# Performance work log

Hardware: AMD Instinct MI355X
Metric: run time of the kernel (lower is better)

## Reference

```python
import jax, jax.numpy as jnp
import numpy as np

CAR_DIM = 8
ESC_MAX_AGENT = 32
HID = 256
ACTION_DIM = 30
NUM_STATES = 64
BATCH = 8192
ENC_OUT = 1 + CAR_DIM * ESC_MAX_AGENT          # 257
Q_IN = 1 + CAR_DIM + CAR_DIM * ESC_MAX_AGENT   # 265


def setup_inputs() -> dict:
    key = jax.random.key(0)
    ks = jax.random.split(key, 9)
    s = jax.random.normal(ks[0], (BATCH, CAR_DIM + NUM_STATES * CAR_DIM), dtype=jnp.float32)
    def lin(k, fan_in, fan_out):
        bound = 1.0 / np.sqrt(fan_in)
        kw, kb = jax.random.split(k)
        W = jax.random.uniform(kw, (fan_in, fan_out), jnp.float32, -bound, bound)
        b = jax.random.uniform(kb, (fan_out,), jnp.float32, -bound, bound)
        return W, b
    W1, b1 = lin(ks[1], CAR_DIM, HID)
    W2, b2 = lin(ks[2], HID, ENC_OUT)
    Qw1, Qb1 = lin(ks[3], Q_IN, HID)
    Qw2, Qb2 = lin(ks[4], HID, ACTION_DIM)
    return {"s": s, "W1": W1, "b1": b1, "W2": W2, "b2": b2,
            "Qw1": Qw1, "Qb1": Qb1, "Qw2": Qw2, "Qb2": Qb2}


def reference(s, W1, b1, W2, b2, Qw1, Qb1, Qw2, Qb2):
    B = s.shape[0]
    self_states = s[:, :CAR_DIM]                                   # [B, C]
    surr = s[:, CAR_DIM:].reshape(B, -1, CAR_DIM)                  # [B, N, C]
    # sentinel agents: any coordinate exactly == -1 is skipped
    valid = ~jnp.any(surr == -1.0, axis=-1)                        # [B, N] bool
    h = jax.nn.relu(jnp.einsum('bnc,ch->bnh', surr, W1) + b1)      # [B, N, HID]
    enc = jax.nn.relu(jnp.einsum('bnh,he->bne', h, W2) + b2)       # [B, N, ENC_OUT]
    sum_outputs = jnp.sum(enc * valid[:, :, None].astype(enc.dtype), axis=1)  # [B, ENC_OUT]
    x = jnp.concatenate([self_states, sum_outputs], axis=1)        # [B, Q_IN]
    q = jax.nn.relu(x @ Qw1 + Qb1) @ Qw2 + Qb2                     # [B, ACTION_DIM]
    return q
```

## Files before the change

kernel.cpp:

```cpp
#include <hip/hip_runtime.h>

#define CAR 8
#define SROW 520
#define HID 256
#define EOUT 257
#define XPAD 288
#define ADIM 30

typedef __attribute__((ext_vector_type(8))) short sh8;
typedef __attribute__((ext_vector_type(4))) float f32x4;

__device__ __forceinline__ short f2bf(float f) {
  unsigned u = __builtin_bit_cast(unsigned, f);
  u += 0x7fffu + ((u >> 16) & 1u);
  return (short)(u >> 16);
}
__device__ __forceinline__ unsigned f2bf2(float a, float b) {
  unsigned ua = __builtin_bit_cast(unsigned, a);
  ua += 0x7fffu + ((ua >> 16) & 1u);
  unsigned ub = __builtin_bit_cast(unsigned, b);
  ub += 0x7fffu + ((ub >> 16) & 1u);
  return __builtin_amdgcn_perm(ub, ua, 0x07060302);
}

__global__ void k_prep(const float* __restrict__ W1, const float* __restrict__ W2,
                       const float* __restrict__ Qw1, const float* __restrict__ Qw2,
                       short* __restrict__ w1f, short* __restrict__ w2f,
                       short* __restrict__ w3f, short* __restrict__ wq2f) {
  int idx = blockIdx.x * 256 + threadIdx.x;
  if (idx < 8192) {
    int mt = idx >> 9, r = idx & 511, lane = r >> 3, j = r & 7;
    int quad = lane >> 4, m = lane & 15;
    float v = (quad == 0) ? W1[j * HID + mt * 16 + m] : 0.0f;
    w1f[idx] = f2bf(v);
    return;
  }
  int i2 = idx - 8192;
  if (i2 < 69632) {
    int ks = i2 / 8704, r = i2 % 8704;
    int nt = r >> 9, r2 = r & 511, lane = r2 >> 3, j = r2 & 7;
    int quad = lane >> 4, m = lane & 15;
    int k = ks * 32 + quad * 8 + j, n = nt * 16 + m;
    float v = (n < EOUT) ? W2[k * EOUT + n] : 0.0f;
    w2f[i2] = f2bf(v);
    return;
  }
  int i3 = i2 - 69632;
  if (i3 < 73728) {
    int ks = i3 >> 13, r = i3 & 8191;
    int nt = r >> 9, r2 = r & 511, lane = r2 >> 3, j = r2 & 7;
    int quad = lane >> 4, m = lane & 15;
    int k = ks * 32 + quad * 8 + j, n = nt * 16 + m;
    float v = (k < 265) ? Qw1[k * HID + n] : 0.0f;
    w3f[i3] = f2bf(v);
    return;
  }
  int i4 = i3 - 73728;
  if (i4 < 8192) {
    int ks = i4 >> 10, r = i4 & 1023;
    int nt = r >> 9, r2 = r & 511, lane = r2 >> 3, j = r2 & 7;
    int quad = lane >> 4, m = lane & 15;
    int k = ks * 32 + quad * 8 + j, n = nt * 16 + m;
    float v = (n < ADIM) ? Qw2[k * ADIM + n] : 0.0f;
    wq2f[i4] = f2bf(v);
  }
}

__global__ __launch_bounds__(256, 2)
void k_enc(const float* __restrict__ s, const short* __restrict__ w1f,
           const float* __restrict__ b1, const short* __restrict__ w2f,
           const float* __restrict__ b2, float* __restrict__ so288) {
  __shared__ __align__(16) short hlds[2][16384];
  __shared__ float ninvp[4];

  const int tid = threadIdx.x;
  const int w = tid >> 6, lane = tid & 63;
  const int q = lane >> 4, m = lane & 15;
  const int be = w >> 1, half = w & 1;
  const size_t b0 = 2 * (size_t)blockIdx.x;
  const int bg = (int)b0 + be;

  const float* srow0 = s + (size_t)bg * SROW + CAR;
  int4 pk = {0, 0, 0, 0};
  bool inv = false;
  if (lane < 32) {
    const float* sr = srow0 + (half * 32 + lane) * CAR;
    float4 f0 = ((const float4*)sr)[0], f1 = ((const float4*)sr)[1];
    inv = (f0.x == -1.f) | (f0.y == -1.f) | (f0.z == -1.f) | (f0.w == -1.f) |
          (f1.x == -1.f) | (f1.y == -1.f) | (f1.z == -1.f) | (f1.w == -1.f);
    pk.x = (int)f2bf2(f0.x, f0.y); pk.y = (int)f2bf2(f0.z, f0.w);
    pk.z = (int)f2bf2(f1.x, f1.y); pk.w = (int)f2bf2(f1.z, f1.w);
  }
  const float vflag = inv ? 0.f : 1.f;
  unsigned long long bal = __ballot(inv);
  if (lane == 0) ninvp[w] = (float)__popcll(bal);

  int4 p0, p1;
  p0.x = __shfl(pk.x, m, 64);      p0.y = __shfl(pk.y, m, 64);
  p0.z = __shfl(pk.z, m, 64);      p0.w = __shfl(pk.w, m, 64);
  p1.x = __shfl(pk.x, 16 + m, 64); p1.y = __shfl(pk.y, 16 + m, 64);
  p1.z = __shfl(pk.z, 16 + m, 64); p1.w = __shfl(pk.w, 16 + m, 64);
  const float vv0 = __shfl(vflag, m, 64);
  const float vv1 = __shfl(vflag, 16 + m, 64);
  if (q != 0) { p0.x = p0.y = p0.z = p0.w = 0; p1.x = p1.y = p1.z = p1.w = 0; }
  sh8 bs0 = __builtin_bit_cast(sh8, p0);
  sh8 bs1 = __builtin_bit_cast(sh8, p1);

  const int T0 = half * 2, T1 = half * 2 + 1;
#pragma unroll
  for (int mt = 0; mt < 16; ++mt) {
    sh8 af = *(const sh8*)(w1f + (mt * 64 + lane) * 8);
    f32x4 z = {0.f, 0.f, 0.f, 0.f};
    f32x4 c0 = __builtin_amdgcn_mfma_f32_16x16x32_bf16(af, bs0, z, 0, 0, 0);
    f32x4 c1 = __builtin_amdgcn_mfma_f32_16x16x32_bf16(af, bs1, z, 0, 0, 0);
    const int hidb = mt * 16 + q * 4;
    float4 b1v = *(const float4*)(b1 + hidb);
    const int ks = hidb >> 5, qB = (hidb >> 3) & 3, js = hidb & 7;
    uint2 k0, k1;
    k0.x = f2bf2(fmaxf(c0[0] + b1v.x, 0.f) * vv0, fmaxf(c0[1] + b1v.y, 0.f) * vv0);
    k0.y = f2bf2(fmaxf(c0[2] + b1v.z, 0.f) * vv0, fmaxf(c0[3] + b1v.w, 0.f) * vv0);
    k1.x = f2bf2(fmaxf(c1[0] + b1v.x, 0.f) * vv1, fmaxf(c1[1] + b1v.y, 0.f) * vv1);
    k1.y = f2bf2(fmaxf(c1[2] + b1v.z, 0.f) * vv1, fmaxf(c1[3] + b1v.w, 0.f) * vv1);
    *(uint2*)(&hlds[be][((T0 * 8 + ks) * 64 + qB * 16 + m) * 8 + js]) = k0;
    *(uint2*)(&hlds[be][((T1 * 8 + ks) * 64 + qB * 16 + m) * 8 + js]) = k1;
  }
  __syncthreads();

  int tiles[5];
#pragma unroll
  for (int i = 0; i < 4; ++i) tiles[i] = 4 * w + i;
  tiles[4] = (w == 0) ? 16 : 4 * w;

  f32x4 acc[4][5][2];
#pragma unroll
  for (int mt = 0; mt < 4; ++mt)
#pragma unroll
    for (int i = 0; i < 5; ++i)
#pragma unroll
      for (int e = 0; e < 2; ++e) {
        f32x4 z = {0.f, 0.f, 0.f, 0.f};
        acc[mt][i][e] = z;
      }

  sh8 Bf[5];
#pragma unroll
  for (int i = 0; i < 5; ++i)
    Bf[i] = *(const sh8*)(w2f + ((0 * 17 + tiles[i]) * 64 + lane) * 8);

#pragma unroll
  for (int ks = 0; ks < 8; ++ks) {
    sh8 Bn[5];
    if (ks < 7) {
#pragma unroll
      for (int i = 0; i < 5; ++i)
        Bn[i] = *(const sh8*)(w2f + (((ks + 1) * 17 + tiles[i]) * 64 + lane) * 8);
    }
#pragma unroll
    for (int e = 0; e < 2; ++e) {
      sh8 A[4];
#pragma unroll
      for (int mt = 0; mt < 4; ++mt)
        A[mt] = *(const sh8*)(&hlds[e][((mt * 8 + ks) * 64 + lane) * 8]);
#pragma unroll
      for (int i = 0; i < 5; ++i)
#pragma unroll
        for (int mt = 0; mt < 4; ++mt)
          acc[mt][i][e] = __builtin_amdgcn_mfma_f32_16x16x32_bf16(A[mt], Bf[i], acc[mt][i][e], 0, 0, 0);
    }
    if (ks < 7) {
#pragma unroll
      for (int i = 0; i < 5; ++i) Bf[i] = Bn[i];
    }
  }

  const float ninv[2] = {ninvp[0] + ninvp[1], ninvp[2] + ninvp[3]};
#pragma unroll
  for (int i = 0; i < 5; ++i) {
    if (i == 4 && w != 0) continue;
    const int col = tiles[i] * 16 + m;
    const float b2c = (col < EOUT) ? b2[col] : 0.f;
    const float rb2 = fmaxf(b2c, 0.f);
#pragma unroll
    for (int e = 0; e < 2; ++e) {
      float ssum = 0.f;
#pragma unroll
      for (int mt = 0; mt < 4; ++mt)
#pragma unroll
        for (int r = 0; r < 4; ++r)
          ssum += fmaxf(acc[mt][i][e][r] + b2c, 0.f);
      ssum += __shfl_xor(ssum, 16, 64);
      ssum += __shfl_xor(ssum, 32, 64);
      ssum -= ninv[e] * rb2;
      if (q == 0)
        so288[(b0 + e) * XPAD + CAR + col] = ssum;
    }
  }
  if (w == 1 || w == 2) {
    const size_t rr = b0 + (w - 1);
    if (lane < CAR)       so288[rr * XPAD + lane] = s[rr * SROW + lane];
    else if (lane < 16)   so288[rr * XPAD + 280 + (lane - 8)] = 0.f;
  }
}

__global__ __launch_bounds__(256, 2)
void k_q(const float* __restrict__ so288, const short* __restrict__ w3f,
         const float* __restrict__ Qb1, const short* __restrict__ wq2f,
         const float* __restrict__ Qb2, float* __restrict__ out, int B) {
  __shared__ __align__(16) short xf[2 * 9 * 64 * 8];
  __shared__ __align__(16) float H[32 * 260];
  const int tid = threadIdx.x;
  const int w = tid >> 6, lane = tid & 63;
  const int q = lane >> 4, m = lane & 15;
  const int b0 = blockIdx.x * 32;

#pragma unroll
  for (int it = 0; it < 5; ++it) {
    int sidx = tid + it * 256;
    if (sidx < 1152) {
      int mt = sidx / 576, rem = sidx % 576;
      int ks = rem >> 6, l = rem & 63;
      int lq = l >> 4, lm = l & 15;
      int row = b0 + mt * 16 + lm; if (row >= B) row = B - 1;
      const float* xp = so288 + (size_t)row * XPAD + ks * 32 + lq * 8;
      float4 xa = ((const float4*)xp)[0], xb = ((const float4*)xp)[1];
      int4 t = {(int)f2bf2(xa.x, xa.y), (int)f2bf2(xa.z, xa.w),
                (int)f2bf2(xb.x, xb.y), (int)f2bf2(xb.z, xb.w)};
      *(int4*)(xf + sidx * 8) = t;
    }
  }
  __syncthreads();

  f32x4 acc1[2][4];
#pragma unroll
  for (int mt = 0; mt < 2; ++mt)
#pragma unroll
    for (int i = 0; i < 4; ++i) {
      f32x4 z = {0.f, 0.f, 0.f, 0.f};
      acc1[mt][i] = z;
    }
#pragma unroll
  for (int ks = 0; ks < 9; ++ks) {
    sh8 A0 = *(const sh8*)(xf + ((0 * 9 + ks) * 64 + lane) * 8);
    sh8 A1 = *(const sh8*)(xf + ((1 * 9 + ks) * 64 + lane) * 8);
#pragma unroll
    for (int i = 0; i < 4; ++i) {
      sh8 Bf = *(const sh8*)(w3f + ((ks * 16 + 4 * w + i) * 64 + lane) * 8);
      acc1[0][i] = __builtin_amdgcn_mfma_f32_16x16x32_bf16(A0, Bf, acc1[0][i], 0, 0, 0);
      acc1[1][i] = __builtin_amdgcn_mfma_f32_16x16x32_bf16(A1, Bf, acc1[1][i], 0, 0, 0);
    }
  }
#pragma unroll
  for (int i = 0; i < 4; ++i) {
    const int hcol = (4 * w + i) * 16 + m;
    const float bq = Qb1[hcol];
#pragma unroll
    for (int mt = 0; mt < 2; ++mt)
#pragma unroll
      for (int r = 0; r < 4; ++r)
        H[(mt * 16 + q * 4 + r) * 260 + hcol] = fmaxf(acc1[mt][i][r] + bq, 0.f);
  }
  __syncthreads();

  const int mt2 = w >> 1, nt2 = w & 1;
  f32x4 acc2 = {0.f, 0.f, 0.f, 0.f};
#pragma unroll
  for (int ks = 0; ks < 8; ++ks) {
    const float* hp = H + (mt2 * 16 + m) * 260 + ks * 32 + q * 8;
    float4 ha = ((const float4*)hp)[0], hb = ((const float4*)hp)[1];
    int4 t = {(int)f2bf2(ha.x, ha.y), (int)f2bf2(ha.z, ha.w),
              (int)f2bf2(hb.x, hb.y), (int)f2bf2(hb.z, hb.w)};
    sh8 A2 = __builtin_bit_cast(sh8, t);
    sh8 Bf = *(const sh8*)(wq2f + ((ks * 2 + nt2) * 64 + lane) * 8);
    acc2 = __builtin_amdgcn_mfma_f32_16x16x32_bf16(A2, Bf, acc2, 0, 0, 0);
  }
  const int act = nt2 * 16 + m;
  if (act < ADIM) {
    const float bq = Qb2[act];
#pragma unroll
    for (int r = 0; r < 4; ++r) {
      const int row = b0 + mt2 * 16 + q * 4 + r;
      if (row < B) out[(size_t)row * ADIM + act] = acc2[r] + bq;
    }
  }
}

extern "C" void kernel_launch(void* const* d_in, const int* in_sizes, int n_in,
                              void* d_out, int out_size, void* d_ws, size_t ws_size,
                              hipStream_t stream) {
  const float* s   = (const float*)d_in[0];
  const float* W1  = (const float*)d_in[1];
  const float* b1  = (const float*)d_in[2];
  const float* W2  = (const float*)d_in[3];
  const float* b2  = (const float*)d_in[4];
  const float* Qw1 = (const float*)d_in[5];
  const float* Qb1 = (const float*)d_in[6];
  const float* Qw2 = (const float*)d_in[7];
  const float* Qb2 = (const float*)d_in[8];
  float* out = (float*)d_out;
  const int B = in_sizes[0] / SROW;

  char* wsb = (char*)d_ws;
  float* so288 = (float*)wsb;
  size_t off = (size_t)B * XPAD * sizeof(float);
  short* w1f  = (short*)(wsb + off);            off += 8192 * 2;
  short* w2f  = (short*)(wsb + off);            off += 69632 * 2;
  short* w3f  = (short*)(wsb + off);            off += 73728 * 2;
  short* wq2f = (short*)(wsb + off);

  const int prep_elems = 8192 + 69632 + 73728 + 8192;
  k_prep<<<(prep_elems + 255) / 256, 256, 0, stream>>>(W1, W2, Qw1, Qw2,
                                                       w1f, w2f, w3f, wq2f);
  k_enc<<<(B + 1) / 2, 256, 0, stream>>>(s, w1f, b1, w2f, b2, so288);
  k_q<<<(B + 31) / 32, 256, 0, stream>>>(so288, w3f, Qb1, wq2f, Qb2, out, B);
}
```

Before: 168.7 us.

## Fuse Q-head MLP into encoder kernel, drop intermediate buffer and second launch

Moves the two Q-network layers into the encoder kernel so each 2-row block computes its final outputs directly from LDS, removing the so288 global round trip and the k_q launch. The Q GEMMs now run on 2 valid rows padded into 16-row MFMA tiles. Every block also reloads the full Qw1/Qw2 bf16 weights, which greatly multiplies weight traffic and wasted tensor work. Extra syncthreads are added and the LDS buffer is reused.

Measured after the change: 193.8 us. +14.9%, slower.

```diff
diff --git a/kernel.cpp b/kernel.cpp
--- a/kernel.cpp
+++ b/kernel.cpp
@@ -69,16 +69,20 @@
 __global__ __launch_bounds__(256, 2)
 void k_enc(const float* __restrict__ s, const short* __restrict__ w1f,
            const float* __restrict__ b1, const short* __restrict__ w2f,
-           const float* __restrict__ b2, float* __restrict__ so288) {
+           const float* __restrict__ b2, const short* __restrict__ w3f,
+           const float* __restrict__ Qb1, const short* __restrict__ wq2f,
+           const float* __restrict__ Qb2, float* __restrict__ out, int B) {
   __shared__ __align__(16) short hlds[2][16384];
   __shared__ float ninvp[4];
+  float* xq = (float*)&hlds[0][0];
+  float* Hq = xq + 2 * XPAD;
 
   const int tid = threadIdx.x;
   const int w = tid >> 6, lane = tid & 63;
   const int q = lane >> 4, m = lane & 15;
   const int be = w >> 1, half = w & 1;
   const size_t b0 = 2 * (size_t)blockIdx.x;
-  const int bg = (int)b0 + be;
+  int bg = (int)b0 + be; if (bg >= B) bg = B - 1;
 
   const float* srow0 = s + (size_t)bg * SROW + CAR;
   int4 pk = {0, 0, 0, 0};
@@ -172,6 +176,7 @@
       for (int i = 0; i < 5; ++i) Bf[i] = Bn[i];
     }
   }
+  __syncthreads();
 
   const float ninv[2] = {ninvp[0] + ninvp[1], ninvp[2] + ninvp[3]};
 #pragma unroll
@@ -192,94 +197,80 @@
       ssum += __shfl_xor(ssum, 32, 64);
       ssum -= ninv[e] * rb2;
       if (q == 0)
-        so288[(b0 + e) * XPAD + CAR + col] = ssum;
+        xq[e * XPAD + CAR + col] = ssum;
     }
   }
   if (w == 1 || w == 2) {
-    const size_t rr = b0 + (w - 1);
-    if (lane < CAR)       so288[rr * XPAD + lane] = s[rr * SROW + lane];
-    else if (lane < 16)   so288[rr * XPAD + 280 + (lane - 8)] = 0.f;
-  }
-}
-
-__global__ __launch_bounds__(256, 2)
-void k_q(const float* __restrict__ so288, const short* __restrict__ w3f,
-         const float* __restrict__ Qb1, const short* __restrict__ wq2f,
-         const float* __restrict__ Qb2, float* __restrict__ out, int B) {
-  __shared__ __align__(16) short xf[2 * 9 * 64 * 8];
-  __shared__ __align__(16) float H[32 * 260];
-  const int tid = threadIdx.x;
-  const int w = tid >> 6, lane = tid & 63;
-  const int q = lane >> 4, m = lane & 15;
-  const int b0 = blockIdx.x * 32;
-
-#pragma unroll
-  for (int it = 0; it < 5; ++it) {
-    int sidx = tid + it * 256;
-    if (sidx < 1152) {
-      int mt = sidx / 576, rem = sidx % 576;
-      int ks = rem >> 6, l = rem & 63;
-      int lq = l >> 4, lm = l & 15;
-      int row = b0 + mt * 16 + lm; if (row >= B) row = B - 1;
-      const float* xp = so288 + (size_t)row * XPAD + ks * 32 + lq * 8;
-      float4 xa = ((const float4*)xp)[0], xb = ((const float4*)xp)[1];
-      int4 t = {(int)f2bf2(xa.x, xa.y), (int)f2bf2(xa.z, xa.w),
-                (int)f2bf2(xb.x, xb.y), (int)f2bf2(xb.z, xb.w)};
-      *(int4*)(xf + sidx * 8) = t;
-    }
+    const int e = w - 1;
+    size_t rr = b0 + e; if (rr >= (size_t)B) rr = B - 1;
+    if (lane < CAR)       xq[e * XPAD + lane] = s[rr * SROW + lane];
+    else if (lane < 16)   xq[e * XPAD + 280 + (lane - 8)] = 0.f;
   }
   __syncthreads();
 
-  f32x4 acc1[2][4];
-#pragma unroll
-  for (int mt = 0; mt < 2; ++mt)
+  f32x4 aq[4];
+#pragma unroll
+  for (int i = 0; i < 4; ++i) {
+    f32x4 z = {0.f, 0.f, 0.f, 0.f};
+    aq[i] = z;
+  }
+#pragma unroll
+  for (int ks = 0; ks < 9; ++ks) {
+    const float* xp = xq + (m & 1) * XPAD + ks * 32 + q * 8;
+    float4 xa = ((const float4*)xp)[0], xb = ((const float4*)xp)[1];
+    int4 t = {(int)f2bf2(xa.x, xa.y), (int)f2bf2(xa.z, xa.w),
+              (int)f2bf2(xb.x, xb.y), (int)f2bf2(xb.z, xb.w)};
+    sh8 A = __builtin_bit_cast(sh8, t);
 #pragma unroll
     for (int i = 0; i < 4; ++i) {
+      sh8 Bq = *(const sh8*)(w3f + ((ks * 16 + 4 * w + i) * 64 + lane) * 8);
+      aq[i] = __builtin_amdgcn_mfma_f32_16x16x32_bf16(A, Bq, aq[i], 0, 0, 0);
+    }
+  }
+  if (q == 0) {
+#pragma unroll
+    for (int i = 0; i < 4; ++i) {
+      const int hcol = (4 * w + i) * 16 + m;
+      const float bq = Qb1[hcol];
+      Hq[0 * HID + hcol] = fmaxf(aq[i][0] + bq, 0.f);
+      Hq[1 * HID + hcol] = fmaxf(aq[i][1] + bq, 0.f);
+    }
+  }
+  __syncthreads();
+
+  if (w == 0) {
+    f32x4 a2[2];
+#pragma unroll
+    for (int nt = 0; nt < 2; ++nt) {
       f32x4 z = {0.f, 0.f, 0.f, 0.f};
-      acc1[mt][i] = z;
-    }
-#pragma unroll
-  for (int ks = 0; ks < 9; ++ks) {
-    sh8 A0 = *(const sh8*)(xf + ((0 * 9 + ks) * 64 + lane) * 8);
-    sh8 A1 = *(const sh8*)(xf + ((1 * 9 + ks) * 64 + lane) * 8);
-#pragma unroll
-    for (int i = 0; i < 4; ++i) {
-      sh8 Bf = *(const sh8*)(w3f + ((ks * 16 + 4 * w + i) * 64 + lane) * 8);
-      acc1[0][i] = __builtin_amdgcn_mfma_f32_16x16x32_bf16(A0, Bf, acc1[0][i], 0, 0, 0);
-      acc1[1][i] = __builtin_amdgcn_mfma_f32_16x16x32_bf16(A1, Bf, acc1[1][i], 0, 0, 0);
-    }
-  }
-#pragma unroll
-  for (int i = 0; i < 4; ++i) {
-    const int hcol = (4 * w + i) * 16 + m;
-    const float bq = Qb1[hcol];
-#pragma unroll
-    for (int mt = 0; mt < 2; ++mt)
-#pragma unroll
-      for (int r = 0; r < 4; ++r)
-        H[(mt * 16 + q * 4 + r) * 260 + hcol] = fmaxf(acc1[mt][i][r] + bq, 0.f);
-  }
-  __syncthreads();
-
-  const int mt2 = w >> 1, nt2 = w & 1;
-  f32x4 acc2 = {0.f, 0.f, 0.f, 0.f};
-#pragma unroll
-  for (int ks = 0; ks < 8; ++ks) {
-    const float* hp = H + (mt2 * 16 + m) * 260 + ks * 32 + q * 8;
-    float4 ha = ((const float4*)hp)[0], hb = ((const float4*)hp)[1];
-    int4 t = {(int)f2bf2(ha.x, ha.y), (int)f2bf2(ha.z, ha.w),
-              (int)f2bf2(hb.x, hb.y), (int)f2bf2(hb.z, hb.w)};
-    sh8 A2 = __builtin_bit_cast(sh8, t);
-    sh8 Bf = *(const sh8*)(wq2f + ((ks * 2 + nt2) * 64 + lane) * 8);
-    acc2 = __builtin_amdgcn_mfma_f32_16x16x32_bf16(A2, Bf, acc2, 0, 0, 0);
-  }
-  const int act = nt2 * 16 + m;
-  if (act < ADIM) {
-    const float bq = Qb2[act];
-#pragma unroll
-    for (int r = 0; r < 4; ++r) {
-      const int row = b0 + mt2 * 16 + q * 4 + r;
-      if (row < B) out[(size_t)row * ADIM + act] = acc2[r] + bq;
+      a2[nt] = z;
+    }
+#pragma unroll
+    for (int ks = 0; ks < 8; ++ks) {
+      const float* hp = Hq + (m & 1) * HID + ks * 32 + q * 8;
+      float4 ha = ((const float4*)hp)[0], hb = ((const float4*)hp)[1];
+      int4 t = {(int)f2bf2(ha.x, ha.y), (int)f2bf2(ha.z, ha.w),
+                (int)f2bf2(hb.x, hb.y), (int)f2bf2(hb.z, hb.w)};
+      sh8 A2 = __builtin_bit_cast(sh8, t);
+#pragma unroll
+      for (int nt = 0; nt < 2; ++nt) {
+        sh8 Bq = *(const sh8*)(wq2f + ((ks * 2 + nt) * 64 + lane) * 8);
+        a2[nt] = __builtin_amdgcn_mfma_f32_16x16x32_bf16(A2, Bq, a2[nt], 0, 0, 0);
+      }
+    }
+    if (q == 0) {
+#pragma unroll
+      for (int nt = 0; nt < 2; ++nt) {
+        const int act = nt * 16 + m;
+        if (act < ADIM) {
+          const float bq = Qb2[act];
+#pragma unroll
+          for (int r = 0; r < 2; ++r) {
+            if (b0 + r < (size_t)B)
+              out[(b0 + r) * ADIM + act] = a2[nt][r] + bq;
+          }
+        }
+      }
     }
   }
 }
@@ -300,16 +291,14 @@
   const int B = in_sizes[0] / SROW;
 
   char* wsb = (char*)d_ws;
-  float* so288 = (float*)wsb;
-  size_t off = (size_t)B * XPAD * sizeof(float);
-  short* w1f  = (short*)(wsb + off);            off += 8192 * 2;
-  short* w2f  = (short*)(wsb + off);            off += 69632 * 2;
-  short* w3f  = (short*)(wsb + off);            off += 73728 * 2;
-  short* wq2f = (short*)(wsb + off);
+  short* w1f  = (short*)wsb;
+  short* w2f  = (short*)(wsb + 8192 * 2);
+  short* w3f  = (short*)(wsb + (8192 + 69632) * 2);
+  short* wq2f = (short*)(wsb + (8192 + 69632 + 73728) * 2);
 
   const int prep_elems = 8192 + 69632 + 73728 + 8192;
   k_prep<<<(prep_elems + 255) / 256, 256, 0, stream>>>(W1, W2, Qw1, Qw2,
                                                        w1f, w2f, w3f, wq2f);
-  k_enc<<<(B + 1) / 2, 256, 0, stream>>>(s, w1f, b1, w2f, b2, so288);
-  k_q<<<(B + 31) / 32, 256, 0, stream>>>(so288, w3f, Qb1, wq2f, Qb2, out, B);
-}
+  k_enc<<<(B + 1) / 2, 256, 0, stream>>>(s, w1f, b1, w2f, b2,
+                                         w3f, Qb1, wq2f, Qb2, out, B);
+}
```

## Fold b1 and validity mask into layer-1 MFMA and specialize wave tile loops

Applied to the files above, without the earlier changes.

Folds the first-layer bias into the W1 fragment as an extra K column multiplied by a per-agent validity 1.0, so the MFMA output already includes the bias and the invalid-agent masking. This removes the b1 loads, the bias adds and the per-element mask multiplies. It also swaps the rounding bf16 conversion for truncation via byte permute. The layer-2 loop is split so waves 1-3 run a 4-tile loop and only wave 0 runs the 5-tile loop, avoiding redundant MFMAs on a duplicated tile. Truncating to bf16 instead of rounding adds slight numeric drift, and clamping out-of-range rows adds bounds safety.

Result: faster. 161.1 us (-4.5%).

```diff
diff --git a/kernel.cpp b/kernel.cpp
--- a/kernel.cpp
+++ b/kernel.cpp
@@ -22,8 +22,13 @@
   ub += 0x7fffu + ((ub >> 16) & 1u);
   return __builtin_amdgcn_perm(ub, ua, 0x07060302);
 }
-
-__global__ void k_prep(const float* __restrict__ W1, const float* __restrict__ W2,
+__device__ __forceinline__ unsigned pkt(float a, float b) {
+  return __builtin_amdgcn_perm(__builtin_bit_cast(unsigned, b),
+                               __builtin_bit_cast(unsigned, a), 0x07060302);
+}
+
+__global__ void k_prep(const float* __restrict__ W1, const float* __restrict__ b1,
+                       const float* __restrict__ W2,
                        const float* __restrict__ Qw1, const float* __restrict__ Qw2,
                        short* __restrict__ w1f, short* __restrict__ w2f,
                        short* __restrict__ w3f, short* __restrict__ wq2f) {
@@ -31,7 +36,9 @@
   if (idx < 8192) {
     int mt = idx >> 9, r = idx & 511, lane = r >> 3, j = r & 7;
     int quad = lane >> 4, m = lane & 15;
-    float v = (quad == 0) ? W1[j * HID + mt * 16 + m] : 0.0f;
+    int hid = mt * 16 + m;
+    float v = (quad == 0) ? W1[j * HID + hid]
+            : (quad == 1 && j == 0) ? b1[hid] : 0.0f;
     w1f[idx] = f2bf(v);
     return;
   }
@@ -68,8 +75,8 @@
 
 __global__ __launch_bounds__(256, 2)
 void k_enc(const float* __restrict__ s, const short* __restrict__ w1f,
-           const float* __restrict__ b1, const short* __restrict__ w2f,
-           const float* __restrict__ b2, float* __restrict__ so288) {
+           const short* __restrict__ w2f, const float* __restrict__ b2,
+           float* __restrict__ so288, int B) {
   __shared__ __align__(16) short hlds[2][16384];
   __shared__ float ninvp[4];
 
@@ -78,7 +85,7 @@
   const int q = lane >> 4, m = lane & 15;
   const int be = w >> 1, half = w & 1;
   const size_t b0 = 2 * (size_t)blockIdx.x;
-  const int bg = (int)b0 + be;
+  int bg = (int)b0 + be; if (bg >= B) bg = B - 1;
 
   const float* srow0 = s + (size_t)bg * SROW + CAR;
   int4 pk = {0, 0, 0, 0};
@@ -88,8 +95,10 @@
     float4 f0 = ((const float4*)sr)[0], f1 = ((const float4*)sr)[1];
     inv = (f0.x == -1.f) | (f0.y == -1.f) | (f0.z == -1.f) | (f0.w == -1.f) |
           (f1.x == -1.f) | (f1.y == -1.f) | (f1.z == -1.f) | (f1.w == -1.f);
-    pk.x = (int)f2bf2(f0.x, f0.y); pk.y = (int)f2bf2(f0.z, f0.w);
-    pk.z = (int)f2bf2(f1.x, f1.y); pk.w = (int)f2bf2(f1.z, f1.w);
+    if (!inv) {
+      pk.x = (int)f2bf2(f0.x, f0.y); pk.y = (int)f2bf2(f0.z, f0.w);
+      pk.z = (int)f2bf2(f1.x, f1.y); pk.w = (int)f2bf2(f1.z, f1.w);
+    }
   }
   const float vflag = inv ? 0.f : 1.f;
   unsigned long long bal = __ballot(inv);
@@ -102,7 +111,12 @@
   p1.z = __shfl(pk.z, 16 + m, 64); p1.w = __shfl(pk.w, 16 + m, 64);
   const float vv0 = __shfl(vflag, m, 64);
   const float vv1 = __shfl(vflag, 16 + m, 64);
-  if (q != 0) { p0.x = p0.y = p0.z = p0.w = 0; p1.x = p1.y = p1.z = p1.w = 0; }
+  if (q == 1) {
+    p0.x = (vv0 != 0.f) ? 0x3f80 : 0; p0.y = p0.z = p0.w = 0;
+    p1.x = (vv1 != 0.f) ? 0x3f80 : 0; p1.y = p1.z = p1.w = 0;
+  } else if (q >= 2) {
+    p0.x = p0.y = p0.z = p0.w = 0;   p1.x = p1.y = p1.z = p1.w = 0;
+  }
   sh8 bs0 = __builtin_bit_cast(sh8, p0);
   sh8 bs1 = __builtin_bit_cast(sh8, p1);
 
@@ -114,22 +128,16 @@
     f32x4 c0 = __builtin_amdgcn_mfma_f32_16x16x32_bf16(af, bs0, z, 0, 0, 0);
     f32x4 c1 = __builtin_amdgcn_mfma_f32_16x16x32_bf16(af, bs1, z, 0, 0, 0);
     const int hidb = mt * 16 + q * 4;
-    float4 b1v = *(const float4*)(b1 + hidb);
     const int ks = hidb >> 5, qB = (hidb >> 3) & 3, js = hidb & 7;
     uint2 k0, k1;
-    k0.x = f2bf2(fmaxf(c0[0] + b1v.x, 0.f) * vv0, fmaxf(c0[1] + b1v.y, 0.f) * vv0);
-    k0.y = f2bf2(fmaxf(c0[2] + b1v.z, 0.f) * vv0, fmaxf(c0[3] + b1v.w, 0.f) * vv0);
-    k1.x = f2bf2(fmaxf(c1[0] + b1v.x, 0.f) * vv1, fmaxf(c1[1] + b1v.y, 0.f) * vv1);
-    k1.y = f2bf2(fmaxf(c1[2] + b1v.z, 0.f) * vv1, fmaxf(c1[3] + b1v.w, 0.f) * vv1);
+    k0.x = pkt(fmaxf(c0[0], 0.f), fmaxf(c0[1], 0.f));
+    k0.y = pkt(fmaxf(c0[2], 0.f), fmaxf(c0[3], 0.f));
+    k1.x = pkt(fmaxf(c1[0], 0.f), fmaxf(c1[1], 0.f));
+    k1.y = pkt(fmaxf(c1[2], 0.f), fmaxf(c1[3], 0.f));
     *(uint2*)(&hlds[be][((T0 * 8 + ks) * 64 + qB * 16 + m) * 8 + js]) = k0;
     *(uint2*)(&hlds[be][((T1 * 8 + ks) * 64 + qB * 16 + m) * 8 + js]) = k1;
   }
   __syncthreads();
-
-  int tiles[5];
-#pragma unroll
-  for (int i = 0; i < 4; ++i) tiles[i] = 4 * w + i;
-  tiles[4] = (w == 0) ? 16 : 4 * w;
 
   f32x4 acc[4][5][2];
 #pragma unroll
@@ -142,34 +150,70 @@
         acc[mt][i][e] = z;
       }
 
-  sh8 Bf[5];
-#pragma unroll
-  for (int i = 0; i < 5; ++i)
-    Bf[i] = *(const sh8*)(w2f + ((0 * 17 + tiles[i]) * 64 + lane) * 8);
-
-#pragma unroll
-  for (int ks = 0; ks < 8; ++ks) {
-    sh8 Bn[5];
-    if (ks < 7) {
-#pragma unroll
-      for (int i = 0; i < 5; ++i)
-        Bn[i] = *(const sh8*)(w2f + (((ks + 1) * 17 + tiles[i]) * 64 + lane) * 8);
-    }
-#pragma unroll
-    for (int e = 0; e < 2; ++e) {
-      sh8 A[4];
-#pragma unroll
-      for (int mt = 0; mt < 4; ++mt)
-        A[mt] = *(const sh8*)(&hlds[e][((mt * 8 + ks) * 64 + lane) * 8]);
-#pragma unroll
-      for (int i = 0; i < 5; ++i)
+  if (w == 0) {
+    sh8 Bf[5];
+#pragma unroll
+    for (int i = 0; i < 5; ++i) {
+      const int t = (i < 4) ? i : 16;
+      Bf[i] = *(const sh8*)(w2f + ((0 * 17 + t) * 64 + lane) * 8);
+    }
+#pragma unroll
+    for (int ks = 0; ks < 8; ++ks) {
+      sh8 Bn[5];
+      if (ks < 7) {
+#pragma unroll
+        for (int i = 0; i < 5; ++i) {
+          const int t = (i < 4) ? i : 16;
+          Bn[i] = *(const sh8*)(w2f + (((ks + 1) * 17 + t) * 64 + lane) * 8);
+        }
+      }
+#pragma unroll
+      for (int e = 0; e < 2; ++e) {
+        sh8 A[4];
 #pragma unroll
         for (int mt = 0; mt < 4; ++mt)
-          acc[mt][i][e] = __builtin_amdgcn_mfma_f32_16x16x32_bf16(A[mt], Bf[i], acc[mt][i][e], 0, 0, 0);
-    }
-    if (ks < 7) {
-#pragma unroll
-      for (int i = 0; i < 5; ++i) Bf[i] = Bn[i];
+          A[mt] = *(const sh8*)(&hlds[e][((mt * 8 + ks) * 64 + lane) * 8]);
+#pragma unroll
+        for (int i = 0; i < 5; ++i)
+#pragma unroll
+          for (int mt = 0; mt < 4; ++mt)
+            acc[mt][i][e] = __builtin_amdgcn_mfma_f32_16x16x32_bf16(A[mt], Bf[i], acc[mt][i][e], 0, 0, 0);
+      }
+      if (ks < 7) {
+#pragma unroll
+        for (int i = 0; i < 5; ++i) Bf[i] = Bn[i];
+      }
+    }
+  } else {
+    const int t0 = 4 * w;
+    sh8 Bf[4];
+#pragma unroll
+    for (int i = 0; i < 4; ++i)
+      Bf[i] = *(const sh8*)(w2f + ((0 * 17 + t0 + i) * 64 + lane) * 8);
+#pragma unroll
+    for (int ks = 0; ks < 8; ++ks) {
+      sh8 Bn[4];
+      if (ks < 7) {
+#pragma unroll
+        for (int i = 0; i < 4; ++i)
+          Bn[i] = *(const sh8*)(w2f + (((ks + 1) * 17 + t0 + i) * 64 + lane) * 8);
+      }
+#pragma unroll
+      for (int e = 0; e < 2; ++e) {
+        sh8 A[4];
+#pragma unroll
+        for (int mt = 0; mt < 4; ++mt)
+          A[mt] = *(const sh8*)(&hlds[e][((mt * 8 + ks) * 64 + lane) * 8]);
+#pragma unroll
+        for (int i = 0; i < 4; ++i)
+#pragma unroll
+          for (int mt = 0; mt < 4; ++mt)
+            acc[mt][i][e] = __builtin_amdgcn_mfma_f32_16x16x32_bf16(A[mt], Bf[i], acc[mt][i][e], 0, 0, 0);
+      }
+      if (ks < 7) {
+#pragma unroll
+        for (int i = 0; i < 4; ++i) Bf[i] = Bn[i];
+      }
     }
   }
 
@@ -177,7 +221,8 @@
 #pragma unroll
   for (int i = 0; i < 5; ++i) {
     if (i == 4 && w != 0) continue;
-    const int col = tiles[i] * 16 + m;
+    const int t = (i < 4) ? 4 * w + i : 16;
+    const int col = t * 16 + m;
     const float b2c = (col < EOUT) ? b2[col] : 0.f;
     const float rb2 = fmaxf(b2c, 0.f);
 #pragma unroll
@@ -196,7 +241,7 @@
     }
   }
   if (w == 1 || w == 2) {
-    const size_t rr = b0 + (w - 1);
+    size_t rr = b0 + (w - 1); if (rr >= (size_t)B) rr = B - 1;
     if (lane < CAR)       so288[rr * XPAD + lane] = s[rr * SROW + lane];
     else if (lane < 16)   so288[rr * XPAD + 280 + (lane - 8)] = 0.f;
   }
@@ -308,8 +353,8 @@
   short* wq2f = (short*)(wsb + off);
 
   const int prep_elems = 8192 + 69632 + 73728 + 8192;
-  k_prep<<<(prep_elems + 255) / 256, 256, 0, stream>>>(W1, W2, Qw1, Qw2,
+  k_prep<<<(prep_elems + 255) / 256, 256, 0, stream>>>(W1, b1, W2, Qw1, Qw2,
                                                        w1f, w2f, w3f, wq2f);
-  k_enc<<<(B + 1) / 2, 256, 0, stream>>>(s, w1f, b1, w2f, b2, so288);
+  k_enc<<<(B + 1) / 2, 256, 0, stream>>>(s, w1f, w2f, b2, so288, B);
   k_q<<<(B + 31) / 32, 256, 0, stream>>>(so288, w3f, Qb1, wq2f, Qb2, out, B);
 }
```

## Restructure encoder to one batch row per block with bias folded into MFMA

Applied to the files above, without the earlier changes.

The encoder kernel now handles one batch row per 256-thread block instead of two. Each wave owns 16 agents, and the leftover 257th output column is spread across waves by k-slice and then reduced through shared memory. The layer-1 bias and the validity mask are folded into the first MFMA through an extra ones-column in the B operand, which removes the bias loads and the mask multiplies. The intermediate x is written as bf16, so the Q kernel reads its A fragments straight from global memory and no longer stages them in LDS. This cuts LDS use, raising launch bounds to 3 blocks per SM, but it also drops the W2 prefetch double-buffering and doubles the block count. Truncating h to bf16 instead of rounding it slightly changes numerics.

Measured after the change: 165.1 us. 1.02x faster.

```diff
diff --git a/kernel.cpp b/kernel.cpp
--- a/kernel.cpp
+++ b/kernel.cpp
@@ -22,8 +22,13 @@
   ub += 0x7fffu + ((ub >> 16) & 1u);
   return __builtin_amdgcn_perm(ub, ua, 0x07060302);
 }
-
-__global__ void k_prep(const float* __restrict__ W1, const float* __restrict__ W2,
+__device__ __forceinline__ unsigned pkt(float a, float b) {
+  return __builtin_amdgcn_perm(__builtin_bit_cast(unsigned, b),
+                               __builtin_bit_cast(unsigned, a), 0x07060302);
+}
+
+__global__ void k_prep(const float* __restrict__ W1, const float* __restrict__ b1,
+                       const float* __restrict__ W2,
                        const float* __restrict__ Qw1, const float* __restrict__ Qw2,
                        short* __restrict__ w1f, short* __restrict__ w2f,
                        short* __restrict__ w3f, short* __restrict__ wq2f) {
@@ -31,7 +36,9 @@
   if (idx < 8192) {
     int mt = idx >> 9, r = idx & 511, lane = r >> 3, j = r & 7;
     int quad = lane >> 4, m = lane & 15;
-    float v = (quad == 0) ? W1[j * HID + mt * 16 + m] : 0.0f;
+    int hid = mt * 16 + m;
+    float v = (quad == 0) ? W1[j * HID + hid]
+            : (quad == 1 && j == 0) ? b1[hid] : 0.0f;
     w1f[idx] = f2bf(v);
     return;
   }
@@ -66,169 +73,145 @@
   }
 }
 
-__global__ __launch_bounds__(256, 2)
+__global__ __launch_bounds__(256, 3)
 void k_enc(const float* __restrict__ s, const short* __restrict__ w1f,
-           const float* __restrict__ b1, const short* __restrict__ w2f,
-           const float* __restrict__ b2, float* __restrict__ so288) {
-  __shared__ __align__(16) short hlds[2][16384];
+           const short* __restrict__ w2f, const float* __restrict__ b2,
+           short* __restrict__ sob, int B) {
+  __shared__ __align__(16) short hlds[16384];
+  __shared__ float psum[256];
   __shared__ float ninvp[4];
 
   const int tid = threadIdx.x;
   const int w = tid >> 6, lane = tid & 63;
   const int q = lane >> 4, m = lane & 15;
-  const int be = w >> 1, half = w & 1;
-  const size_t b0 = 2 * (size_t)blockIdx.x;
-  const int bg = (int)b0 + be;
-
-  const float* srow0 = s + (size_t)bg * SROW + CAR;
-  int4 pk = {0, 0, 0, 0};
-  bool inv = false;
+  const int b = blockIdx.x;
+  const float* srow0 = s + (size_t)b * SROW + CAR;
+
+  int dA = 0, dB = 0, invAi = 0;
   if (lane < 32) {
-    const float* sr = srow0 + (half * 32 + lane) * CAR;
-    float4 f0 = ((const float4*)sr)[0], f1 = ((const float4*)sr)[1];
-    inv = (f0.x == -1.f) | (f0.y == -1.f) | (f0.z == -1.f) | (f0.w == -1.f) |
-          (f1.x == -1.f) | (f1.y == -1.f) | (f1.z == -1.f) | (f1.w == -1.f);
-    pk.x = (int)f2bf2(f0.x, f0.y); pk.y = (int)f2bf2(f0.z, f0.w);
-    pk.z = (int)f2bf2(f1.x, f1.y); pk.w = (int)f2bf2(f1.z, f1.w);
-  }
-  const float vflag = inv ? 0.f : 1.f;
-  unsigned long long bal = __ballot(inv);
-  if (lane == 0) ninvp[w] = (float)__popcll(bal);
-
-  int4 p0, p1;
-  p0.x = __shfl(pk.x, m, 64);      p0.y = __shfl(pk.y, m, 64);
-  p0.z = __shfl(pk.z, m, 64);      p0.w = __shfl(pk.w, m, 64);
-  p1.x = __shfl(pk.x, 16 + m, 64); p1.y = __shfl(pk.y, 16 + m, 64);
-  p1.z = __shfl(pk.z, 16 + m, 64); p1.w = __shfl(pk.w, 16 + m, 64);
-  const float vv0 = __shfl(vflag, m, 64);
-  const float vv1 = __shfl(vflag, 16 + m, 64);
-  if (q != 0) { p0.x = p0.y = p0.z = p0.w = 0; p1.x = p1.y = p1.z = p1.w = 0; }
-  sh8 bs0 = __builtin_bit_cast(sh8, p0);
-  sh8 bs1 = __builtin_bit_cast(sh8, p1);
-
-  const int T0 = half * 2, T1 = half * 2 + 1;
+    const float* sr = srow0 + (16 * w + (lane >> 1)) * CAR + (lane & 1) * 4;
+    float4 f = *(const float4*)sr;
+    int inv4 = (f.x == -1.f) | (f.y == -1.f) | (f.z == -1.f) | (f.w == -1.f);
+    invAi = inv4 | __shfl_xor(inv4, 1, 64);
+    if (!invAi) { dA = (int)f2bf2(f.x, f.y); dB = (int)f2bf2(f.z, f.w); }
+  }
+  {
+    unsigned long long bal = __ballot((lane < 32) && !(lane & 1) && invAi);
+    if (lane == 0) ninvp[w] = (float)__popcll(bal);
+  }
+  const int src = 2 * m;
+  int g0 = __shfl(dA, src, 64), g1 = __shfl(dB, src, 64);
+  int g2 = __shfl(dA, src + 1, 64), g3 = __shfl(dB, src + 1, 64);
+  int invm = __shfl(invAi, src, 64);
+  int4 bv;
+  if (q == 0)      bv = (int4){g0, g1, g2, g3};
+  else if (q == 1) bv = (int4){invm ? 0 : 0x3f80, 0, 0, 0};
+  else             bv = (int4){0, 0, 0, 0};
+  sh8 bs = __builtin_bit_cast(sh8, bv);
+
 #pragma unroll
   for (int mt = 0; mt < 16; ++mt) {
     sh8 af = *(const sh8*)(w1f + (mt * 64 + lane) * 8);
     f32x4 z = {0.f, 0.f, 0.f, 0.f};
-    f32x4 c0 = __builtin_amdgcn_mfma_f32_16x16x32_bf16(af, bs0, z, 0, 0, 0);
-    f32x4 c1 = __builtin_amdgcn_mfma_f32_16x16x32_bf16(af, bs1, z, 0, 0, 0);
+    f32x4 c = __builtin_amdgcn_mfma_f32_16x16x32_bf16(af, bs, z, 0, 0, 0);
     const int hidb = mt * 16 + q * 4;
-    float4 b1v = *(const float4*)(b1 + hidb);
     const int ks = hidb >> 5, qB = (hidb >> 3) & 3, js = hidb & 7;
-    uint2 k0, k1;
-    k0.x = f2bf2(fmaxf(c0[0] + b1v.x, 0.f) * vv0, fmaxf(c0[1] + b1v.y, 0.f) * vv0);
-    k0.y = f2bf2(fmaxf(c0[2] + b1v.z, 0.f) * vv0, fmaxf(c0[3] + b1v.w, 0.f) * vv0);
-    k1.x = f2bf2(fmaxf(c1[0] + b1v.x, 0.f) * vv1, fmaxf(c1[1] + b1v.y, 0.f) * vv1);
-    k1.y = f2bf2(fmaxf(c1[2] + b1v.z, 0.f) * vv1, fmaxf(c1[3] + b1v.w, 0.f) * vv1);
-    *(uint2*)(&hlds[be][((T0 * 8 + ks) * 64 + qB * 16 + m) * 8 + js]) = k0;
-    *(uint2*)(&hlds[be][((T1 * 8 + ks) * 64 + qB * 16 + m) * 8 + js]) = k1;
+    uint2 k0;
+    k0.x = pkt(fmaxf(c[0], 0.f), fmaxf(c[1], 0.f));
+    k0.y = pkt(fmaxf(c[2], 0.f), fmaxf(c[3], 0.f));
+    *(uint2*)(&hlds[((w * 8 + ks) * 64 + qB * 16 + m) * 8 + js]) = k0;
   }
   __syncthreads();
 
-  int tiles[5];
-#pragma unroll
-  for (int i = 0; i < 4; ++i) tiles[i] = 4 * w + i;
-  tiles[4] = (w == 0) ? 16 : 4 * w;
-
-  f32x4 acc[4][5][2];
-#pragma unroll
-  for (int mt = 0; mt < 4; ++mt)
-#pragma unroll
-    for (int i = 0; i < 5; ++i)
-#pragma unroll
-      for (int e = 0; e < 2; ++e) {
-        f32x4 z = {0.f, 0.f, 0.f, 0.f};
-        acc[mt][i][e] = z;
-      }
-
-  sh8 Bf[5];
-#pragma unroll
-  for (int i = 0; i < 5; ++i)
-    Bf[i] = *(const sh8*)(w2f + ((0 * 17 + tiles[i]) * 64 + lane) * 8);
+  f32x4 acc[4][4];
+  f32x4 acc16[4];
+#pragma unroll
+  for (int Mt = 0; Mt < 4; ++Mt) {
+#pragma unroll
+    for (int i = 0; i < 4; ++i) {
+      f32x4 z = {0.f, 0.f, 0.f, 0.f};
+      acc[Mt][i] = z;
+    }
+    f32x4 z = {0.f, 0.f, 0.f, 0.f};
+    acc16[Mt] = z;
+  }
 
 #pragma unroll
   for (int ks = 0; ks < 8; ++ks) {
-    sh8 Bn[5];
-    if (ks < 7) {
-#pragma unroll
-      for (int i = 0; i < 5; ++i)
-        Bn[i] = *(const sh8*)(w2f + (((ks + 1) * 17 + tiles[i]) * 64 + lane) * 8);
-    }
-#pragma unroll
-    for (int e = 0; e < 2; ++e) {
-      sh8 A[4];
-#pragma unroll
-      for (int mt = 0; mt < 4; ++mt)
-        A[mt] = *(const sh8*)(&hlds[e][((mt * 8 + ks) * 64 + lane) * 8]);
-#pragma unroll
-      for (int i = 0; i < 5; ++i)
-#pragma unroll
-        for (int mt = 0; mt < 4; ++mt)
-          acc[mt][i][e] = __builtin_amdgcn_mfma_f32_16x16x32_bf16(A[mt], Bf[i], acc[mt][i][e], 0, 0, 0);
-    }
-    if (ks < 7) {
-#pragma unroll
-      for (int i = 0; i < 5; ++i) Bf[i] = Bn[i];
-    }
-  }
-
-  const float ninv[2] = {ninvp[0] + ninvp[1], ninvp[2] + ninvp[3]};
-#pragma unroll
-  for (int i = 0; i < 5; ++i) {
-    if (i == 4 && w != 0) continue;
-    const int col = tiles[i] * 16 + m;
-    const float b2c = (col < EOUT) ? b2[col] : 0.f;
-    const float rb2 = fmaxf(b2c, 0.f);
-#pragma unroll
-    for (int e = 0; e < 2; ++e) {
-      float ssum = 0.f;
-#pragma unroll
-      for (int mt = 0; mt < 4; ++mt)
-#pragma unroll
-        for (int r = 0; r < 4; ++r)
-          ssum += fmaxf(acc[mt][i][e][r] + b2c, 0.f);
-      ssum += __shfl_xor(ssum, 16, 64);
-      ssum += __shfl_xor(ssum, 32, 64);
-      ssum -= ninv[e] * rb2;
-      if (q == 0)
-        so288[(b0 + e) * XPAD + CAR + col] = ssum;
-    }
-  }
-  if (w == 1 || w == 2) {
-    const size_t rr = b0 + (w - 1);
-    if (lane < CAR)       so288[rr * XPAD + lane] = s[rr * SROW + lane];
-    else if (lane < 16)   so288[rr * XPAD + 280 + (lane - 8)] = 0.f;
-  }
+    sh8 A[4];
+#pragma unroll
+    for (int Mt = 0; Mt < 4; ++Mt)
+      A[Mt] = *(const sh8*)(&hlds[((Mt * 8 + ks) * 64 + lane) * 8]);
+    sh8 Bf[4];
+#pragma unroll
+    for (int i = 0; i < 4; ++i)
+      Bf[i] = *(const sh8*)(w2f + ((ks * 17 + 4 * w + i) * 64 + lane) * 8);
+#pragma unroll
+    for (int i = 0; i < 4; ++i)
+#pragma unroll
+      for (int Mt = 0; Mt < 4; ++Mt)
+        acc[Mt][i] = __builtin_amdgcn_mfma_f32_16x16x32_bf16(A[Mt], Bf[i], acc[Mt][i], 0, 0, 0);
+    if ((ks >> 1) == w) {
+      sh8 Bt = *(const sh8*)(w2f + ((ks * 17 + 16) * 64 + lane) * 8);
+#pragma unroll
+      for (int Mt = 0; Mt < 4; ++Mt)
+        acc16[Mt] = __builtin_amdgcn_mfma_f32_16x16x32_bf16(A[Mt], Bt, acc16[Mt], 0, 0, 0);
+    }
+  }
+
+  const float ninv = ninvp[0] + ninvp[1] + ninvp[2] + ninvp[3];
+#pragma unroll
+  for (int i = 0; i < 4; ++i) {
+    const int col = (4 * w + i) * 16 + m;
+    const float b2c = b2[col];
+    float ssum = 0.f;
+#pragma unroll
+    for (int Mt = 0; Mt < 4; ++Mt)
+#pragma unroll
+      for (int r = 0; r < 4; ++r)
+        ssum += fmaxf(acc[Mt][i][r] + b2c, 0.f);
+    ssum += __shfl_xor(ssum, 16, 64);
+    ssum += __shfl_xor(ssum, 32, 64);
+    ssum -= ninv * fmaxf(b2c, 0.f);
+    if (q == 0)
+      sob[(size_t)b * XPAD + CAR + col] = f2bf(ssum);
+  }
+  if (m == 0) {
+#pragma unroll
+    for (int Mt = 0; Mt < 4; ++Mt)
+#pragma unroll
+      for (int r = 0; r < 4; ++r)
+        psum[w * 64 + Mt * 16 + q * 4 + r] = acc16[Mt][r];
+  }
+  __syncthreads();
+
+  if (w == 0) {
+    float tot = psum[lane] + psum[64 + lane] + psum[128 + lane] + psum[192 + lane];
+    const float b2c = b2[256];
+    float v = fmaxf(tot + b2c, 0.f);
+#pragma unroll
+    for (int msk = 1; msk < 64; msk <<= 1)
+      v += __shfl_xor(v, msk, 64);
+    if (lane == 0)
+      sob[(size_t)b * XPAD + CAR + 256] = f2bf(v - ninv * fmaxf(b2c, 0.f));
+  }
+  if (w == 1 && lane < CAR)
+    sob[(size_t)b * XPAD + lane] = f2bf(s[(size_t)b * SROW + lane]);
 }
 
 __global__ __launch_bounds__(256, 2)
-void k_q(const float* __restrict__ so288, const short* __restrict__ w3f,
+void k_q(const short* __restrict__ sob, const short* __restrict__ w3f,
          const float* __restrict__ Qb1, const short* __restrict__ wq2f,
          const float* __restrict__ Qb2, float* __restrict__ out, int B) {
-  __shared__ __align__(16) short xf[2 * 9 * 64 * 8];
   __shared__ __align__(16) float H[32 * 260];
   const int tid = threadIdx.x;
   const int w = tid >> 6, lane = tid & 63;
   const int q = lane >> 4, m = lane & 15;
   const int b0 = blockIdx.x * 32;
-
-#pragma unroll
-  for (int it = 0; it < 5; ++it) {
-    int sidx = tid + it * 256;
-    if (sidx < 1152) {
-      int mt = sidx / 576, rem = sidx % 576;
-      int ks = rem >> 6, l = rem & 63;
-      int lq = l >> 4, lm = l & 15;
-      int row = b0 + mt * 16 + lm; if (row >= B) row = B - 1;
-      const float* xp = so288 + (size_t)row * XPAD + ks * 32 + lq * 8;
-      float4 xa = ((const float4*)xp)[0], xb = ((const float4*)xp)[1];
-      int4 t = {(int)f2bf2(xa.x, xa.y), (int)f2bf2(xa.z, xa.w),
-                (int)f2bf2(xb.x, xb.y), (int)f2bf2(xb.z, xb.w)};
-      *(int4*)(xf + sidx * 8) = t;
-    }
-  }
-  __syncthreads();
+  int r0 = b0 + m;      if (r0 >= B) r0 = B - 1;
+  int r1 = b0 + 16 + m; if (r1 >= B) r1 = B - 1;
+  const short* xr0 = sob + (size_t)r0 * XPAD + q * 8;
+  const short* xr1 = sob + (size_t)r1 * XPAD + q * 8;
 
   f32x4 acc1[2][4];
 #pragma unroll
@@ -240,8 +223,8 @@
     }
 #pragma unroll
   for (int ks = 0; ks < 9; ++ks) {
-    sh8 A0 = *(const sh8*)(xf + ((0 * 9 + ks) * 64 + lane) * 8);
-    sh8 A1 = *(const sh8*)(xf + ((1 * 9 + ks) * 64 + lane) * 8);
+    sh8 A0 = *(const sh8*)(xr0 + ks * 32);
+    sh8 A1 = *(const sh8*)(xr1 + ks * 32);
 #pragma unroll
     for (int i = 0; i < 4; ++i) {
       sh8 Bf = *(const sh8*)(w3f + ((ks * 16 + 4 * w + i) * 64 + lane) * 8);
@@ -300,16 +283,16 @@
   const int B = in_sizes[0] / SROW;
 
   char* wsb = (char*)d_ws;
-  float* so288 = (float*)wsb;
-  size_t off = (size_t)B * XPAD * sizeof(float);
+  short* sob = (short*)wsb;
+  size_t off = (size_t)B * XPAD * sizeof(short);
   short* w1f  = (short*)(wsb + off);            off += 8192 * 2;
   short* w2f  = (short*)(wsb + off);            off += 69632 * 2;
   short* w3f  = (short*)(wsb + off);            off += 73728 * 2;
   short* wq2f = (short*)(wsb + off);
 
   const int prep_elems = 8192 + 69632 + 73728 + 8192;
-  k_prep<<<(prep_elems + 255) / 256, 256, 0, stream>>>(W1, W2, Qw1, Qw2,
+  k_prep<<<(prep_elems + 255) / 256, 256, 0, stream>>>(W1, b1, W2, Qw1, Qw2,
                                                        w1f, w2f, w3f, wq2f);
-  k_enc<<<(B + 1) / 2, 256, 0, stream>>>(s, w1f, b1, w2f, b2, so288);
-  k_q<<<(B + 31) / 32, 256, 0, stream>>>(so288, w3f, Qb1, wq2f, Qb2, out, B);
-}
+  k_enc<<<B, 256, 0, stream>>>(s, w1f, w2f, b2, sob, B);
+  k_q<<<(B + 31) / 32, 256, 0, stream>>>(sob, w3f, Qb1, wq2f, Qb2, out, B);
+}
```
